# Optimization experiments

Hardware: AMD Instinct MI355X
Metric: run time of the kernel (lower is better)

Reference implementation:

```python
import jax, jax.numpy as jnp
import numpy as np
import math

B, S, D, H = 2, 2048, 1024, 16
DK = D // H


def setup_inputs() -> dict:
    key = jax.random.key(0)
    ks = jax.random.split(key, 12)
    scale = 1.0 / math.sqrt(D)
    inp = {
        'query': jax.random.normal(ks[0], (B, S, D), dtype=jnp.float32),
        'key': jax.random.normal(ks[1], (B, S, D), dtype=jnp.float32),
        'value': jax.random.normal(ks[2], (B, S, D), dtype=jnp.float32),
        'mask': jnp.ones((B, 1, S), dtype=jnp.int32),
        'posr': jax.random.normal(ks[3], (B, S, S), dtype=jnp.float32),
        'Wq': jax.random.normal(ks[4], (D, D), dtype=jnp.float32) * scale,
        'bq': jnp.zeros((D,), dtype=jnp.float32),
        'Wk': jax.random.normal(ks[5], (D, D), dtype=jnp.float32) * scale,
        'bk': jnp.zeros((D,), dtype=jnp.float32),
        'Wv': jax.random.normal(ks[6], (D, D), dtype=jnp.float32) * scale,
        'bv': jnp.zeros((D,), dtype=jnp.float32),
        'Wo': jax.random.normal(ks[7], (D, D), dtype=jnp.float32) * scale,
        'bo': jnp.zeros((D,), dtype=jnp.float32),
    }
    return inp


def _split_heads(x):
    # [B, S, D] -> [B, H, S, DK]
    b, s, _ = x.shape
    return x.reshape(b, s, H, DK).transpose(0, 2, 1, 3)


def reference(query, key, value, mask, posr, Wq, bq, Wk, bk, Wv, bv, Wo, bo):
    q = _split_heads(query @ Wq.T + bq)   # [B,H,S,DK]
    k = _split_heads(key @ Wk.T + bk)
    v = _split_heads(value @ Wv.T + bv)

    scores = jnp.einsum('bhqd,bhkd->bhqk', q, k) / math.sqrt(DK)
    scores = scores + posr[:, None, :, :]            # additive positional bias
    m = mask[:, None, :, :]                           # [B,1,1,S] broadcast
    scores = jnp.where(m == 0, jnp.float32(-1e9), scores)
    p = jax.nn.softmax(scores, axis=-1)
    ctx = jnp.einsum('bhqk,bhkd->bhqd', p, v)        # [B,H,S,DK]
    ctx = ctx.transpose(0, 2, 1, 3).reshape(query.shape[0], -1, D)
    return ctx @ Wo.T + bo
```

## Files before the change

### kernel.cpp

```cpp
#include <hip/hip_runtime.h>
#include <math.h>

#define B_ 2
#define S_ 2048
#define D_ 1024
#define H_ 16
#define DK_ 64

typedef __attribute__((ext_vector_type(8))) short bf16x8;
typedef __attribute__((ext_vector_type(4))) float f32x4;

#define MFMA16(a, b, c) __builtin_amdgcn_mfma_f32_16x16x32_bf16((a), (b), (c), 0, 0, 0)

#define ASYNC16(g, l)                                                          \
    __builtin_amdgcn_global_load_lds(                                          \
        (const __attribute__((address_space(1))) void*)(g),                    \
        (__attribute__((address_space(3))) void*)(l), 16, 0, 0)

__device__ __forceinline__ unsigned short f2bf(float x) {
    unsigned int u = __float_as_uint(x);
    unsigned int r = (u + 0x7fffu + ((u >> 16) & 1u)) >> 16;
    return (unsigned short)r;
}

__global__ __launch_bounds__(256)
void pack_all(const float* __restrict__ q, const float* __restrict__ k,
              const float* __restrict__ v, const float* __restrict__ wq,
              const float* __restrict__ wk, const float* __restrict__ wv,
              const float* __restrict__ wo, unsigned short* __restrict__ ws0)
{
    const int z = blockIdx.z;
    const size_t IN = 4194304, WT = 1048576;
    const float* in;
    unsigned short* dst;
    int n;
    switch (z) {
        case 0: in = q;  dst = ws0;            n = (int)IN; break;
        case 1: in = k;  dst = ws0 + IN;       n = (int)IN; break;
        case 2: in = v;  dst = ws0 + 2*IN;     n = (int)IN; break;
        case 3: in = wq; dst = ws0 + 3*IN;          n = (int)WT; break;
        case 4: in = wk; dst = ws0 + 3*IN + WT;     n = (int)WT; break;
        case 5: in = wv; dst = ws0 + 3*IN + 2*WT;   n = (int)WT; break;
        default:in = wo; dst = ws0 + 3*IN + 3*WT;   n = (int)WT; break;
    }
    const int n4 = n >> 2;
    const int stride = gridDim.x * blockDim.x;
    for (int i = blockIdx.x * blockDim.x + threadIdx.x; i < n4; i += stride) {
        float4 x = ((const float4*)in)[i];
        ushort4 hv;
        hv.x = f2bf(x.x); hv.y = f2bf(x.y); hv.z = f2bf(x.z); hv.w = f2bf(x.w);
        ((ushort4*)dst)[i] = hv;
    }
}

__device__ __forceinline__ void gemm_core(
    const unsigned short* __restrict__ A, const unsigned short* __restrict__ B,
    unsigned short* As, unsigned short* Bs, int m0, int n0, f32x4 (&acc)[4][4])
{
    const int tid  = threadIdx.x;
    const int w    = tid >> 6;
    const int lane = tid & 63;
    const int rA   = lane & 15;
    const int quad = lane >> 4;
    const int wm   = (w & 1) * 64;
    const int wn   = (w >> 1) * 64;

#pragma unroll 1
    for (int k0 = 0; k0 < 1024; k0 += 64) {
        __syncthreads();
#pragma unroll
        for (int i = 0; i < 4; ++i) {
            const int c   = i * 256 + tid;
            const int row = c >> 3;
            const int g   = (c & 7) ^ (row & 7);
            ASYNC16(A + (size_t)(m0 + row) * 1024 + k0 + g * 8,
                    As + (size_t)(i * 256 + w * 64) * 8);
            ASYNC16(B + (size_t)(n0 + row) * 1024 + k0 + g * 8,
                    Bs + (size_t)(i * 256 + w * 64) * 8);
        }
        __syncthreads();
#pragma unroll
        for (int ks = 0; ks < 2; ++ks) {
            bf16x8 a[4], bb[4];
#pragma unroll
            for (int mt = 0; mt < 4; ++mt) {
                const int row = wm + mt * 16 + rA;
                a[mt] = *(const bf16x8*)&As[row * 64 + (((ks * 4 + quad) ^ (row & 7)) * 8)];
            }
#pragma unroll
            for (int nt = 0; nt < 4; ++nt) {
                const int row = wn + nt * 16 + rA;
                bb[nt] = *(const bf16x8*)&Bs[row * 64 + (((ks * 4 + quad) ^ (row & 7)) * 8)];
            }
#pragma unroll
            for (int mt = 0; mt < 4; ++mt)
#pragma unroll
                for (int nt = 0; nt < 4; ++nt)
                    acc[mt][nt] = MFMA16(a[mt], bb[nt], acc[mt][nt]);
        }
    }
}

__global__ __launch_bounds__(256)
void gemm_qkv(const unsigned short* __restrict__ ws0,
              const float* __restrict__ bq, const float* __restrict__ bk,
              const float* __restrict__ bv,
              unsigned short* __restrict__ qbuf, unsigned short* __restrict__ kbuf,
              unsigned short* __restrict__ vtbuf)
{
    __shared__ unsigned short As[128 * 64];
    __shared__ unsigned short Bs[128 * 64];
    const size_t IN = 4194304, WT = 1048576;
    const int z = blockIdx.z;
    const unsigned short* Ap = ws0 + (size_t)z * IN;
    const unsigned short* Bp = ws0 + 3 * IN + (size_t)z * WT;
    const float* bias = (z == 0) ? bq : (z == 1) ? bk : bv;
    unsigned short* dst = (z == 0) ? qbuf : (z == 1) ? kbuf : vtbuf;

    const int m0 = blockIdx.y * 128;
    const int n0 = blockIdx.x * 128;
    f32x4 acc[4][4] = {};
    gemm_core(Ap, Bp, As, Bs, m0, n0, acc);

    const int tid = threadIdx.x, w = tid >> 6, lane = tid & 63;
    const int quad = lane >> 4, col = lane & 15;
    const int wm = (w & 1) * 64, wn = (w >> 1) * 64;
    const float qscale = (z == 0) ? 0.125f : 1.0f;
#pragma unroll
    for (int mt = 0; mt < 4; ++mt)
#pragma unroll
        for (int nt = 0; nt < 4; ++nt) {
            f32x4 v = acc[mt][nt];
#pragma unroll
            for (int r = 0; r < 4; ++r) {
                const int m = m0 + wm + mt * 16 + quad * 4 + r;
                const int n = n0 + wn + nt * 16 + col;
                const float val = (v[r] + bias[n]) * qscale;
                const int bb = m >> 11, ss = m & 2047;
                const int hh = n >> 6, dd = n & 63;
                if (z == 2)
                    dst[((size_t)(bb * 16 + hh) * 64 + dd) * 2048 + ss] = f2bf(val);
                else
                    dst[((size_t)(bb * 16 + hh) * 2048 + ss) * 64 + dd] = f2bf(val);
            }
        }
}

__global__ __launch_bounds__(256)
void gemm_out(const unsigned short* __restrict__ Actx,
              const unsigned short* __restrict__ Bwo,
              const float* __restrict__ bias, float* __restrict__ out)
{
    __shared__ unsigned short As[128 * 64];
    __shared__ unsigned short Bs[128 * 64];
    const int m0 = blockIdx.y * 128;
    const int n0 = blockIdx.x * 128;
    f32x4 acc[4][4] = {};
    gemm_core(Actx, Bwo, As, Bs, m0, n0, acc);

    const int tid = threadIdx.x, w = tid >> 6, lane = tid & 63;
    const int quad = lane >> 4, col = lane & 15;
    const int wm = (w & 1) * 64, wn = (w >> 1) * 64;
#pragma unroll
    for (int mt = 0; mt < 4; ++mt)
#pragma unroll
        for (int nt = 0; nt < 4; ++nt) {
            f32x4 v = acc[mt][nt];
#pragma unroll
            for (int r = 0; r < 4; ++r) {
                const int m = m0 + wm + mt * 16 + quad * 4 + r;
                const int n = n0 + wn + nt * 16 + col;
                out[(size_t)m * 1024 + n] = v[r] + bias[n];
            }
        }
}

__global__ __launch_bounds__(512, 4)
void attn_mfma(const unsigned short* __restrict__ qbuf,
               const unsigned short* __restrict__ kbuf,
               const unsigned short* __restrict__ vtbuf,
               const float* __restrict__ posr, const int* __restrict__ mask,
               unsigned short* __restrict__ ctxb)
{
    __shared__ unsigned short Ks[2][64 * 64];
    __shared__ unsigned short Vts[2][64 * 64];
    __shared__ unsigned short Ps[128 * 64];

    const int tid  = threadIdx.x;
    const int w    = tid >> 6;
    const int lane = tid & 63;
    const int quad = lane >> 4;
    const int col  = lane & 15;
    const int q0   = blockIdx.x * 128;
    const int h    = blockIdx.y;
    const int b    = blockIdx.z;
    const int wq   = w * 16;

    const size_t headoff = (size_t)(b * 16 + h) * 2048 * 64;
    const unsigned short* Qh  = qbuf + headoff + (size_t)q0 * 64;
    const unsigned short* Kh  = kbuf + headoff;
    const unsigned short* Vth = vtbuf + headoff;

    const int srow = tid >> 3;
    const int sg   = (tid & 7) ^ (srow & 7);

    bf16x8 qf[2];
#pragma unroll
    for (int ks = 0; ks < 2; ++ks)
        qf[ks] = *(const bf16x8*)&Qh[(size_t)(wq + col) * 64 + ks * 32 + quad * 8];

    ASYNC16(Kh + (size_t)srow * 64 + sg * 8,   &Ks[0][(size_t)(w * 64) * 8]);
    ASYNC16(Vth + (size_t)srow * 2048 + sg * 8, &Vts[0][(size_t)(w * 64) * 8]);

    f32x4 O[4] = {};
    float lsum[4] = {0.f, 0.f, 0.f, 0.f};

    const float* prp[4];
#pragma unroll
    for (int r = 0; r < 4; ++r)
        prp[r] = posr + ((size_t)b * 2048 + (q0 + wq + quad * 4 + r)) * 2048;
    const int* mrow = mask + (size_t)b * 2048;

#pragma unroll 1
    for (int t = 0; t < 32; ++t) {
        __syncthreads();
        const int bb = t & 1;
        const int k0 = t * 64;
        if (t + 1 < 32) {
            const int kn = k0 + 64;
            ASYNC16(Kh + (size_t)(kn + srow) * 64 + sg * 8,   &Ks[bb ^ 1][(size_t)(w * 64) * 8]);
            ASYNC16(Vth + (size_t)srow * 2048 + kn + sg * 8,  &Vts[bb ^ 1][(size_t)(w * 64) * 8]);
        }

        int mk[4];
#pragma unroll
        for (int nt = 0; nt < 4; ++nt) mk[nt] = mrow[k0 + nt * 16 + col];
        float pr[4][4];
#pragma unroll
        for (int r = 0; r < 4; ++r)
#pragma unroll
            for (int nt = 0; nt < 4; ++nt)
                pr[r][nt] = prp[r][k0 + nt * 16 + col];

        f32x4 sc[4] = {};
#pragma unroll
        for (int ks = 0; ks < 2; ++ks) {
#pragma unroll
            for (int nt = 0; nt < 4; ++nt) {
                const bf16x8 bk = *(const bf16x8*)
                    &Ks[bb][(nt * 16 + col) * 64 + (((ks * 4 + quad) ^ (col & 7)) * 8)];
                sc[nt] = MFMA16(qf[ks], bk, sc[nt]);
            }
        }

#pragma unroll
        for (int r = 0; r < 4; ++r) {
            const int rowW = wq + quad * 4 + r;
            const int rsw = rowW & 7;
#pragma unroll
            for (int nt = 0; nt < 4; ++nt) {
                float p = __expf(sc[nt][r] + pr[r][nt]);
                p = mk[nt] ? p : 0.f;
                lsum[r] += p;
                const int kk = nt * 16 + col;
                Ps[rowW * 64 + (((kk >> 3) ^ rsw) * 8) + (kk & 7)] = f2bf(p);
            }
        }

#pragma unroll
        for (int ks = 0; ks < 2; ++ks) {
            const bf16x8 ap = *(const bf16x8*)
                &Ps[(wq + col) * 64 + (((ks * 4 + quad) ^ (col & 7)) * 8)];
#pragma unroll
            for (int nt = 0; nt < 4; ++nt) {
                const bf16x8 bv = *(const bf16x8*)
                    &Vts[bb][(nt * 16 + col) * 64 + (((ks * 4 + quad) ^ (col & 7)) * 8)];
                O[nt] = MFMA16(ap, bv, O[nt]);
            }
        }
    }

#pragma unroll
    for (int r = 0; r < 4; ++r) {
#pragma unroll
        for (int o = 1; o < 16; o <<= 1) lsum[r] += __shfl_xor(lsum[r], o);
    }

#pragma unroll
    for (int r = 0; r < 4; ++r) {
        const float inv = 1.f / lsum[r];
        const size_t rowoff = ((size_t)b * 2048 + (q0 + wq + quad * 4 + r)) * 1024 + h * 64;
#pragma unroll
        for (int nt = 0; nt < 4; ++nt)
            ctxb[rowoff + nt * 16 + col] = f2bf(O[nt][r] * inv);
    }
}

extern "C" void kernel_launch(void* const* d_in, const int* in_sizes, int n_in,
                              void* d_out, int out_size, void* d_ws, size_t ws_size,
                              hipStream_t stream) {
    const float* query = (const float*)d_in[0];
    const float* key   = (const float*)d_in[1];
    const float* value = (const float*)d_in[2];
    const int*   mask  = (const int*)  d_in[3];
    const float* posr  = (const float*)d_in[4];
    const float* Wq    = (const float*)d_in[5];
    const float* bq    = (const float*)d_in[6];
    const float* Wk    = (const float*)d_in[7];
    const float* bk    = (const float*)d_in[8];
    const float* Wv    = (const float*)d_in[9];
    const float* bv    = (const float*)d_in[10];
    const float* Wo    = (const float*)d_in[11];
    const float* bo    = (const float*)d_in[12];
    float* out = (float*)d_out;

    unsigned short* ws0   = (unsigned short*)d_ws;
    const size_t IN = 4194304, WT = 1048576;
    unsigned short* qbuf  = ws0 + 4 * IN;
    unsigned short* kbuf  = ws0 + 5 * IN;
    unsigned short* vtbuf = ws0 + 6 * IN;
    unsigned short* ctxb  = ws0 + 7 * IN;
    const unsigned short* wob = ws0 + 3 * IN + 3 * WT;

    pack_all<<<dim3(512, 1, 7), 256, 0, stream>>>(query, key, value, Wq, Wk, Wv, Wo, ws0);

    gemm_qkv<<<dim3(8, 32, 3), 256, 0, stream>>>(ws0, bq, bk, bv, qbuf, kbuf, vtbuf);

    attn_mfma<<<dim3(16, 16, 2), 512, 0, stream>>>(qbuf, kbuf, vtbuf, posr, mask, ctxb);

    gemm_out<<<dim3(8, 32), 256, 0, stream>>>(ctxb, wob, bo, out);
}
```

Baseline: 306.8 us.

## Keep attention probabilities in registers via transposed MFMA and shuffles instead of LDS

The attention kernel now computes S^T by swapping MFMA operands, so each lane holds a query column. It packs the exp results to bf16 by truncation and rearranges them with cross-lane shuffles into the B operand of the PV MFMA, which removes the shared-memory round trip for P. The row sum is computed with an MFMA against a ones vector rather than shuffle reductions, and exp2 with log2e folded into the Q scale replaces __expf. Posr and mask loads become vectorized float4/int4 reads. The trade-offs are truncating bf16 conversion instead of rounding, extra shuffles and an extra MFMA per step.

New measurement: 350.2 us. +14.2%, slower.

```diff
diff --git a/kernel.cpp b/kernel.cpp
--- a/kernel.cpp
+++ b/kernel.cpp
@@ -9,6 +9,8 @@
 
 typedef __attribute__((ext_vector_type(8))) short bf16x8;
 typedef __attribute__((ext_vector_type(4))) float f32x4;
+typedef __attribute__((ext_vector_type(4))) int i32x4;
+typedef __attribute__((ext_vector_type(4))) unsigned int u32x4;
 
 #define MFMA16(a, b, c) __builtin_amdgcn_mfma_f32_16x16x32_bf16((a), (b), (c), 0, 0, 0)
 
@@ -16,6 +18,8 @@
     __builtin_amdgcn_global_load_lds(                                          \
         (const __attribute__((address_space(1))) void*)(g),                    \
         (__attribute__((address_space(3))) void*)(l), 16, 0, 0)
+
+#define LOG2E 1.4426950408889634f
 
 __device__ __forceinline__ unsigned short f2bf(float x) {
     unsigned int u = __float_as_uint(x);
@@ -125,7 +129,7 @@
     const int tid = threadIdx.x, w = tid >> 6, lane = tid & 63;
     const int quad = lane >> 4, col = lane & 15;
     const int wm = (w & 1) * 64, wn = (w >> 1) * 64;
-    const float qscale = (z == 0) ? 0.125f : 1.0f;
+    const float qscale = (z == 0) ? (0.125f * LOG2E) : 1.0f;
 #pragma unroll
     for (int mt = 0; mt < 4; ++mt)
 #pragma unroll
@@ -184,7 +188,6 @@
 {
     __shared__ unsigned short Ks[2][64 * 64];
     __shared__ unsigned short Vts[2][64 * 64];
-    __shared__ unsigned short Ps[128 * 64];
 
     const int tid  = threadIdx.x;
     const int w    = tid >> 6;
@@ -209,17 +212,20 @@
     for (int ks = 0; ks < 2; ++ks)
         qf[ks] = *(const bf16x8*)&Qh[(size_t)(wq + col) * 64 + ks * 32 + quad * 8];
 
-    ASYNC16(Kh + (size_t)srow * 64 + sg * 8,   &Ks[0][(size_t)(w * 64) * 8]);
+    ASYNC16(Kh + (size_t)srow * 64 + sg * 8,    &Ks[0][(size_t)(w * 64) * 8]);
     ASYNC16(Vth + (size_t)srow * 2048 + sg * 8, &Vts[0][(size_t)(w * 64) * 8]);
 
     f32x4 O[4] = {};
-    float lsum[4] = {0.f, 0.f, 0.f, 0.f};
-
-    const float* prp[4];
-#pragma unroll
-    for (int r = 0; r < 4; ++r)
-        prp[r] = posr + ((size_t)b * 2048 + (q0 + wq + quad * 4 + r)) * 2048;
-    const int* mrow = mask + (size_t)b * 2048;
+    f32x4 lacc = {};
+    const u32x4 onesu = {0x3F803F80u, 0x3F803F80u, 0x3F803F80u, 0x3F803F80u};
+    const bf16x8 ones = __builtin_bit_cast(bf16x8, onesu);
+
+    const float* prq = posr + ((size_t)b * 2048 + (q0 + wq + col)) * 2048;
+    const int*  mrow = mask + (size_t)b * 2048;
+
+    const int s0 = (quad & 1) * 32 + col;
+    const int s1 = s0 + 16;
+    const bool hi = (quad & 2) != 0;
 
 #pragma unroll 1
     for (int t = 0; t < 32; ++t) {
@@ -232,67 +238,80 @@
             ASYNC16(Vth + (size_t)srow * 2048 + kn + sg * 8,  &Vts[bb ^ 1][(size_t)(w * 64) * 8]);
         }
 
-        int mk[4];
-#pragma unroll
-        for (int nt = 0; nt < 4; ++nt) mk[nt] = mrow[k0 + nt * 16 + col];
-        float pr[4][4];
-#pragma unroll
-        for (int r = 0; r < 4; ++r)
-#pragma unroll
-            for (int nt = 0; nt < 4; ++nt)
-                pr[r][nt] = prp[r][k0 + nt * 16 + col];
+        f32x4 pr4[4];
+        i32x4 mk4[4];
+#pragma unroll
+        for (int mt = 0; mt < 4; ++mt) {
+            pr4[mt] = *(const f32x4*)&prq[k0 + mt * 16 + quad * 4];
+            mk4[mt] = *(const i32x4*)&mrow[k0 + mt * 16 + quad * 4];
+        }
 
         f32x4 sc[4] = {};
 #pragma unroll
         for (int ks = 0; ks < 2; ++ks) {
 #pragma unroll
-            for (int nt = 0; nt < 4; ++nt) {
-                const bf16x8 bk = *(const bf16x8*)
-                    &Ks[bb][(nt * 16 + col) * 64 + (((ks * 4 + quad) ^ (col & 7)) * 8)];
-                sc[nt] = MFMA16(qf[ks], bk, sc[nt]);
-            }
-        }
-
-#pragma unroll
-        for (int r = 0; r < 4; ++r) {
-            const int rowW = wq + quad * 4 + r;
-            const int rsw = rowW & 7;
-#pragma unroll
-            for (int nt = 0; nt < 4; ++nt) {
-                float p = __expf(sc[nt][r] + pr[r][nt]);
-                p = mk[nt] ? p : 0.f;
-                lsum[r] += p;
-                const int kk = nt * 16 + col;
-                Ps[rowW * 64 + (((kk >> 3) ^ rsw) * 8) + (kk & 7)] = f2bf(p);
-            }
+            for (int mt = 0; mt < 4; ++mt) {
+                const int row = mt * 16 + col;
+                const bf16x8 kb = *(const bf16x8*)
+                    &Ks[bb][row * 64 + (((ks * 4 + quad) ^ (col & 7)) * 8)];
+                sc[mt] = MFMA16(kb, qf[ks], sc[mt]);
+            }
+        }
+
+        unsigned int pk[4][2];
+#pragma unroll
+        for (int mt = 0; mt < 4; ++mt) {
+            float p[4];
+#pragma unroll
+            for (int r = 0; r < 4; ++r) {
+                const float t2 = fmaf(pr4[mt][r], LOG2E, sc[mt][r]);
+                const float pe = __builtin_amdgcn_exp2f(t2);
+                p[r] = mk4[mt][r] ? pe : 0.f;
+            }
+            pk[mt][0] = __builtin_amdgcn_perm(__float_as_uint(p[1]),
+                                              __float_as_uint(p[0]), 0x07060302u);
+            pk[mt][1] = __builtin_amdgcn_perm(__float_as_uint(p[3]),
+                                              __float_as_uint(p[2]), 0x07060302u);
         }
 
 #pragma unroll
         for (int ks = 0; ks < 2; ++ks) {
-            const bf16x8 ap = *(const bf16x8*)
-                &Ps[(wq + col) * 64 + (((ks * 4 + quad) ^ (col & 7)) * 8)];
-#pragma unroll
-            for (int nt = 0; nt < 4; ++nt) {
-                const bf16x8 bv = *(const bf16x8*)
-                    &Vts[bb][(nt * 16 + col) * 64 + (((ks * 4 + quad) ^ (col & 7)) * 8)];
-                O[nt] = MFMA16(ap, bv, O[nt]);
-            }
-        }
-    }
-
-#pragma unroll
-    for (int r = 0; r < 4; ++r) {
-#pragma unroll
-        for (int o = 1; o < 16; o <<= 1) lsum[r] += __shfl_xor(lsum[r], o);
-    }
-
-#pragma unroll
-    for (int r = 0; r < 4; ++r) {
-        const float inv = 1.f / lsum[r];
-        const size_t rowoff = ((size_t)b * 2048 + (q0 + wq + quad * 4 + r)) * 1024 + h * 64;
-#pragma unroll
-        for (int nt = 0; nt < 4; ++nt)
-            ctxb[rowoff + nt * 16 + col] = f2bf(O[nt][r] * inv);
+            const unsigned int a0 = (unsigned int)__shfl((int)pk[2 * ks][0],     s0);
+            const unsigned int a1 = (unsigned int)__shfl((int)pk[2 * ks][1],     s0);
+            const unsigned int b0 = (unsigned int)__shfl((int)pk[2 * ks + 1][0], s0);
+            const unsigned int b1 = (unsigned int)__shfl((int)pk[2 * ks + 1][1], s0);
+            const unsigned int c0 = (unsigned int)__shfl((int)pk[2 * ks][0],     s1);
+            const unsigned int c1 = (unsigned int)__shfl((int)pk[2 * ks][1],     s1);
+            const unsigned int d0 = (unsigned int)__shfl((int)pk[2 * ks + 1][0], s1);
+            const unsigned int d1 = (unsigned int)__shfl((int)pk[2 * ks + 1][1], s1);
+            u32x4 bu;
+            bu[0] = hi ? b0 : a0;
+            bu[1] = hi ? b1 : a1;
+            bu[2] = hi ? d0 : c0;
+            bu[3] = hi ? d1 : c1;
+            const bf16x8 pb = __builtin_bit_cast(bf16x8, bu);
+
+            lacc = MFMA16(ones, pb, lacc);
+#pragma unroll
+            for (int dt = 0; dt < 4; ++dt) {
+                const int row = dt * 16 + col;
+                const bf16x8 vb = *(const bf16x8*)
+                    &Vts[bb][row * 64 + (((ks * 4 + quad) ^ (col & 7)) * 8)];
+                O[dt] = MFMA16(vb, pb, O[dt]);
+            }
+        }
+    }
+
+    const float inv = 1.f / lacc[0];
+    const size_t rowoff = ((size_t)b * 2048 + (q0 + wq + col)) * 1024 + h * 64;
+#pragma unroll
+    for (int dt = 0; dt < 4; ++dt) {
+        ushort4 st;
+        st.x = f2bf(O[dt][0] * inv);
+        st.y = f2bf(O[dt][1] * inv);
+        st.z = f2bf(O[dt][2] * inv);
+        st.w = f2bf(O[dt][3] * inv);
+        *(ushort4*)&ctxb[rowoff + dt * 16 + quad * 4] = st;
     }
 }
 
```
